# Optimization experiments

Measured on AMD Instinct MI355X. Metric: run time of the kernel, lower is better.

The kernel has to match this reference:

```python
import jax, jax.numpy as jnp
import numpy as np

N_NODES = 100000
N_EDGES = 1600000
IN_DIM = 128
HID = 64


def setup_inputs() -> dict:
    key = jax.random.key(0)
    ks = jax.random.split(key, 12)
    s = 1.0 / np.sqrt(IN_DIM)
    sh = 1.0 / np.sqrt(HID)
    return {
        "x": jax.random.normal(ks[0], (N_NODES, IN_DIM), jnp.float32),
        "edge_index": jax.random.randint(ks[1], (2, N_EDGES), 0, N_NODES, jnp.int64)
        if jax.config.jax_enable_x64 else jax.random.randint(ks[1], (2, N_EDGES), 0, N_NODES, jnp.int32),
        "edge_attr": jax.random.uniform(ks[2], (N_EDGES, 1), jnp.float32),
        "Wi": jax.random.normal(ks[3], (IN_DIM, HID), jnp.float32) * s,
        "bi": jnp.zeros((HID,), jnp.float32),
        "W1": jax.random.normal(ks[4], (HID, HID), jnp.float32) * sh,
        "b1": jnp.zeros((HID,), jnp.float32),
        "W2": jax.random.normal(ks[5], (HID, HID), jnp.float32) * sh,
        "b2": jnp.zeros((HID,), jnp.float32),
        "W3": jax.random.normal(ks[6], (HID, HID), jnp.float32) * sh,
        "b3": jnp.zeros((HID,), jnp.float32),
    }


def reference(x, edge_index, edge_attr, Wi, bi, W1, b1, W2, b2, W3, b3):
    src = edge_index[0]
    tgt = edge_index[1]
    w = edge_attr[:, 0:1]  # [E,1]
    h = jax.nn.relu(x @ Wi + bi)  # [N,H]
    states = [h]
    for W, b in ((W1, b1), (W2, b2), (W3, b3)):
        # per-edge weighted message, scatter-add into target nodes
        msgs = jax.ops.segment_sum(h[src] * w, tgt, num_segments=h.shape[0])
        h = jax.nn.relu((h + msgs) @ W + b)
        states.append(h)
    return jnp.stack(states)  # [4, N, H] (list of states in the original)
```

## Files before the change

### kernel.cpp

```cpp
#include <hip/hip_runtime.h>
#include <hip/hip_bf16.h>

#define N_NODES 100000
#define N_EDGES 1600000
#define IN_DIM  128
#define HID     64
#define CAP_N   64

#define PITCH_IN  152
#define PITCH_HID 88

typedef __attribute__((ext_vector_type(8))) short bf16x8;
typedef __attribute__((ext_vector_type(4))) float f32x4;

__device__ inline unsigned short f2bf(float f) {
    __hip_bfloat16 b = __float2bfloat16(f);
    return *reinterpret_cast<unsigned short*>(&b);
}

__global__ void wf_prep_kernel(const float* __restrict__ Wi,
                               const float* __restrict__ W1,
                               const float* __restrict__ W2,
                               const float* __restrict__ W3,
                               unsigned short* __restrict__ wf_in,
                               unsigned short* __restrict__ wf_hid,
                               int* __restrict__ cnt) {
    int t = blockIdx.x * 256 + threadIdx.x;
    if (t < N_NODES) cnt[t] = 0;
    if (t < 8192) {
        int j = t & 7, n16 = (t >> 3) & 15, quad = (t >> 7) & 3, nt = (t >> 9) & 3, kc = t >> 11;
        int k = kc * 32 + quad * 8 + j, n = nt * 16 + n16;
        wf_in[t] = f2bf(Wi[k * HID + n]);
    }
    if (t < 4096) {
        int j = t & 7, n16 = (t >> 3) & 15, quad = (t >> 7) & 3, nt = (t >> 9) & 3, kc = t >> 11;
        int k = kc * 32 + quad * 8 + j, n = nt * 16 + n16;
        wf_hid[t]        = f2bf(W1[k * HID + n]);
        wf_hid[4096 + t] = f2bf(W2[k * HID + n]);
        wf_hid[8192 + t] = f2bf(W3[k * HID + n]);
    }
}

__global__ __launch_bounds__(256) void scatter_direct_kernel(
        const int* __restrict__ src,
        const int* __restrict__ tgt,
        const float* __restrict__ ea,
        int* __restrict__ cnt,
        int2* __restrict__ binned) {
    int e = blockIdx.x * 256 + threadIdx.x;
    if (e < N_EDGES) {
        int t = tgt[e];
        int r = atomicAdd(&cnt[t], 1);
        if (r < CAP_N)
            binned[(size_t)t * CAP_N + r] = make_int2(src[e], __float_as_int(ea[e]));
    }
}

__global__ __launch_bounds__(256) void gemm_in_kernel(
        const float* __restrict__ x,
        const unsigned short* __restrict__ wf,
        const float* __restrict__ bi,
        float* __restrict__ h0,
        __hip_bfloat16* __restrict__ hbf) {
    __shared__ unsigned short sX[64 * PITCH_IN];
    const int tid  = threadIdx.x;
    const int row0 = blockIdx.x * 64;

    #pragma unroll
    for (int it = 0; it < 8; ++it) {
        int i  = tid + it * 256;
        int r  = i >> 5;
        int kq = i & 31;
        int rg = row0 + r;
        float4 v = (rg < N_NODES)
                 ? ((const float4*)x)[(size_t)rg * (IN_DIM / 4) + kq]
                 : make_float4(0.f, 0.f, 0.f, 0.f);
        ushort4 pk;
        pk.x = f2bf(v.x); pk.y = f2bf(v.y); pk.z = f2bf(v.z); pk.w = f2bf(v.w);
        *(ushort4*)(sX + r * PITCH_IN + kq * 4) = pk;
    }
    __syncthreads();

    const int lane = tid & 63;
    const int wid  = tid >> 6;
    const int l16  = lane & 15;
    const int q    = lane >> 4;

    f32x4 acc[4] = {{0,0,0,0},{0,0,0,0},{0,0,0,0},{0,0,0,0}};
    const bf16x8* wf8 = (const bf16x8*)wf;

    #pragma unroll
    for (int kc = 0; kc < 4; ++kc) {
        bf16x8 af = *(const bf16x8*)(sX + (wid * 16 + l16) * PITCH_IN + kc * 32 + q * 8);
        #pragma unroll
        for (int nt = 0; nt < 4; ++nt) {
            bf16x8 bfr = wf8[((kc * 4 + nt) * 4 + q) * 16 + l16];
            acc[nt] = __builtin_amdgcn_mfma_f32_16x16x32_bf16(af, bfr, acc[nt], 0, 0, 0);
        }
    }

    #pragma unroll
    for (int nt = 0; nt < 4; ++nt) {
        float bb = bi[nt * 16 + l16];
        #pragma unroll
        for (int reg = 0; reg < 4; ++reg) {
            int rg = row0 + wid * 16 + q * 4 + reg;
            if (rg < N_NODES) {
                float v = fmaxf(acc[nt][reg] + bb, 0.0f);
                h0 [(size_t)rg * HID + nt * 16 + l16] = v;
                hbf[(size_t)rg * HID + nt * 16 + l16] = __float2bfloat16(v);
            }
        }
    }
}

__global__ __launch_bounds__(256) void agg_gemm_kernel(
        const float* __restrict__ h,
        const __hip_bfloat16* __restrict__ hbf_in,
        const int* __restrict__ cnt,
        const int2* __restrict__ binned,
        const unsigned short* __restrict__ wf,
        const float* __restrict__ b,
        float* __restrict__ hnext,
        __hip_bfloat16* __restrict__ hbf_out,
        const int store_bf) {
    __shared__ unsigned short sXs[64 * PITCH_HID];
    const int tid  = threadIdx.x;
    const int row0 = blockIdx.x * 64;
    const int lane = tid & 63;
    const int wid  = tid >> 6;
    const int grp  = lane >> 4;
    const int sub  = lane & 15;

    const int node0 = row0 + wid * 16;

    int cv = 0;
    {
        int nl = node0 + (lane & 15);
        if (lane < 16 && nl < N_NODES) cv = min(cnt[nl], CAP_N);
    }

    int c0 = __shfl(cv, 0);
    int2 pl = binned[(size_t)min(node0, N_NODES - 1) * CAP_N + min(lane, max(c0 - 1, 0))];

    for (int t = 0; t < 16; ++t) {
        const int node = node0 + t;
        const int ccur = __shfl(cv, t);
        const int2 pl_cur = pl;
        if (t < 15) {
            int cn = __shfl(cv, t + 1);
            pl = binned[(size_t)min(node + 1, N_NODES - 1) * CAP_N
                        + min(lane, max(cn - 1, 0))];
        }
        if (node < N_NODES) {
            float ax = 0.f, ay = 0.f, az = 0.f, aw = 0.f;
            const int last = ccur - 1;
            for (int i = 0; i < ccur; i += 8) {
                int e0 = i + grp;
                int e1 = i + 4 + grp;
                bool l0 = (e0 <= last);
                bool l1 = (e1 <= last);
                int s0  = __shfl(pl_cur.x, l0 ? e0 : last);
                int w0i = __shfl(pl_cur.y, l0 ? e0 : last);
                int s1  = __shfl(pl_cur.x, l1 ? e1 : last);
                int w1i = __shfl(pl_cur.y, l1 ? e1 : last);
                uint2 g0 = *(const uint2*)(hbf_in + (size_t)s0 * HID + sub * 4);
                uint2 g1 = *(const uint2*)(hbf_in + (size_t)s1 * HID + sub * 4);
                float w0 = l0 ? __int_as_float(w0i) : 0.0f;
                float w1 = l1 ? __int_as_float(w1i) : 0.0f;
                ax += w0 * __uint_as_float(g0.x << 16);
                ay += w0 * __uint_as_float(g0.x & 0xFFFF0000u);
                az += w0 * __uint_as_float(g0.y << 16);
                aw += w0 * __uint_as_float(g0.y & 0xFFFF0000u);
                ax += w1 * __uint_as_float(g1.x << 16);
                ay += w1 * __uint_as_float(g1.x & 0xFFFF0000u);
                az += w1 * __uint_as_float(g1.y << 16);
                aw += w1 * __uint_as_float(g1.y & 0xFFFF0000u);
            }
            ax += __shfl_xor(ax, 16); ay += __shfl_xor(ay, 16);
            az += __shfl_xor(az, 16); aw += __shfl_xor(aw, 16);
            ax += __shfl_xor(ax, 32); ay += __shfl_xor(ay, 32);
            az += __shfl_xor(az, 32); aw += __shfl_xor(aw, 32);
            if (grp == 0) {
                const float4 hv = *(const float4*)(h + (size_t)node * HID + sub * 4);
                ushort4 pk;
                pk.x = f2bf(hv.x + ax); pk.y = f2bf(hv.y + ay);
                pk.z = f2bf(hv.z + az); pk.w = f2bf(hv.w + aw);
                *(ushort4*)(sXs + (wid * 16 + t) * PITCH_HID + sub * 4) = pk;
            }
        } else if (grp == 0) {
            ushort4 z; z.x = 0; z.y = 0; z.z = 0; z.w = 0;
            *(ushort4*)(sXs + (wid * 16 + t) * PITCH_HID + sub * 4) = z;
        }
    }
    __syncthreads();

    const int l16 = lane & 15;
    const int q   = lane >> 4;

    f32x4 acc[4] = {{0,0,0,0},{0,0,0,0},{0,0,0,0},{0,0,0,0}};
    const bf16x8* wf8 = (const bf16x8*)wf;

    #pragma unroll
    for (int kc = 0; kc < 2; ++kc) {
        bf16x8 af = *(const bf16x8*)(sXs + (wid * 16 + l16) * PITCH_HID + kc * 32 + q * 8);
        #pragma unroll
        for (int nt = 0; nt < 4; ++nt) {
            bf16x8 bfr = wf8[((kc * 4 + nt) * 4 + q) * 16 + l16];
            acc[nt] = __builtin_amdgcn_mfma_f32_16x16x32_bf16(af, bfr, acc[nt], 0, 0, 0);
        }
    }

    #pragma unroll
    for (int nt = 0; nt < 4; ++nt) {
        float bb = b[nt * 16 + l16];
        #pragma unroll
        for (int reg = 0; reg < 4; ++reg) {
            int rg = row0 + wid * 16 + q * 4 + reg;
            if (rg < N_NODES) {
                float v = fmaxf(acc[nt][reg] + bb, 0.0f);
                hnext[(size_t)rg * HID + nt * 16 + l16] = v;
                if (store_bf)
                    hbf_out[(size_t)rg * HID + nt * 16 + l16] = __float2bfloat16(v);
            }
        }
    }
}

extern "C" void kernel_launch(void* const* d_in, const int* in_sizes, int n_in,
                              void* d_out, int out_size, void* d_ws, size_t ws_size,
                              hipStream_t stream) {
    const float* x   = (const float*)d_in[0];
    const int*   ei  = (const int*)  d_in[1];
    const float* ea  = (const float*)d_in[2];
    const float* Wi  = (const float*)d_in[3];
    const float* bi  = (const float*)d_in[4];
    const float* W1  = (const float*)d_in[5];
    const float* b1  = (const float*)d_in[6];
    const float* W2  = (const float*)d_in[7];
    const float* b2  = (const float*)d_in[8];
    const float* W3  = (const float*)d_in[9];
    const float* b3  = (const float*)d_in[10];
    const float* bl[3] = { b1, b2, b3 };
    float* out = (float*)d_out;

    const int* src = ei;
    const int* tgt = ei + N_EDGES;

    int2* binned = (int2*)d_ws;
    int* cnt = (int*)(binned + (size_t)N_NODES * CAP_N);
    __hip_bfloat16* hbf0 = (__hip_bfloat16*)(cnt + N_NODES);
    __hip_bfloat16* hbf1 = hbf0 + (size_t)N_NODES * HID;
    unsigned short* wf_in  = (unsigned short*)(hbf1 + (size_t)N_NODES * HID);
    unsigned short* wf_hid = wf_in + 8192;

    const int prep_blocks = (N_NODES + 255) / 256;
    wf_prep_kernel<<<prep_blocks, 256, 0, stream>>>(Wi, W1, W2, W3,
                                                    wf_in, wf_hid, cnt);

    const int sc_blocks = (N_EDGES + 255) / 256;
    scatter_direct_kernel<<<sc_blocks, 256, 0, stream>>>(src, tgt, ea, cnt, binned);

    const int gemm_blocks = (N_NODES + 63) / 64;
    gemm_in_kernel<<<gemm_blocks, 256, 0, stream>>>(x, wf_in, bi, out, hbf0);

    __hip_bfloat16* hin  = hbf0;
    __hip_bfloat16* hout = hbf1;
    for (int l = 0; l < 3; ++l) {
        const float* hl = out + (size_t)l * N_NODES * HID;
        float* hn       = out + (size_t)(l + 1) * N_NODES * HID;
        agg_gemm_kernel<<<gemm_blocks, 256, 0, stream>>>(
            hl, hin, cnt, binned,
            wf_hid + (size_t)l * 4096, bl[l], hn, hout, (l < 2) ? 1 : 0);
        __hip_bfloat16* t = hin; hin = hout; hout = t;
    }
}
```

Measured before the change: 409.5 us.

## Fuse edge scatter with input GEMM and pad atomic counters

Merges the edge-binning scatter and the input projection GEMM into one launch. Even blocks bin 1024 edges each and odd blocks compute 64 rows of the GEMM, so the atomic-bound scatter can overlap with the bandwidth-bound GEMM. The per-node counters are spread to a 16-int stride so that atomics on neighbouring targets fall on separate cache lines. In exchange, the counter array grows, and the zeroing and later count reads become strided rather than contiguous.

```diff
diff --git a/kernel.cpp b/kernel.cpp
--- a/kernel.cpp
+++ b/kernel.cpp
@@ -6,6 +6,11 @@
 #define IN_DIM  128
 #define HID     64
 #define CAP_N   64
+#define CNT_STRIDE 16
+
+#define SC_EB   1024
+#define SC_BLOCKS ((N_EDGES + SC_EB - 1) / SC_EB)
+#define GEMM_BLOCKS ((N_NODES + 63) / 64)
 
 #define PITCH_IN  152
 #define PITCH_HID 88
@@ -26,7 +31,7 @@
                                unsigned short* __restrict__ wf_hid,
                                int* __restrict__ cnt) {
     int t = blockIdx.x * 256 + threadIdx.x;
-    if (t < N_NODES) cnt[t] = 0;
+    if (t < N_NODES) cnt[(size_t)t * CNT_STRIDE] = 0;
     if (t < 8192) {
         int j = t & 7, n16 = (t >> 3) & 15, quad = (t >> 7) & 3, nt = (t >> 9) & 3, kc = t >> 11;
         int k = kc * 32 + quad * 8 + j, n = nt * 16 + n16;
@@ -41,30 +46,38 @@
     }
 }
 
-__global__ __launch_bounds__(256) void scatter_direct_kernel(
+__global__ __launch_bounds__(256) void fused_scatter_gemm_kernel(
         const int* __restrict__ src,
         const int* __restrict__ tgt,
         const float* __restrict__ ea,
         int* __restrict__ cnt,
-        int2* __restrict__ binned) {
-    int e = blockIdx.x * 256 + threadIdx.x;
-    if (e < N_EDGES) {
-        int t = tgt[e];
-        int r = atomicAdd(&cnt[t], 1);
-        if (r < CAP_N)
-            binned[(size_t)t * CAP_N + r] = make_int2(src[e], __float_as_int(ea[e]));
-    }
-}
-
-__global__ __launch_bounds__(256) void gemm_in_kernel(
+        int2* __restrict__ binned,
         const float* __restrict__ x,
         const unsigned short* __restrict__ wf,
         const float* __restrict__ bi,
         float* __restrict__ h0,
         __hip_bfloat16* __restrict__ hbf) {
     __shared__ unsigned short sX[64 * PITCH_IN];
-    const int tid  = threadIdx.x;
-    const int row0 = blockIdx.x * 64;
+    const int tid = threadIdx.x;
+
+    if ((blockIdx.x & 1) == 0) {
+        const int s  = blockIdx.x >> 1;
+        const int e0 = s * SC_EB;
+        #pragma unroll
+        for (int k = 0; k < SC_EB / 256; ++k) {
+            int e = e0 + tid + k * 256;
+            if (e < N_EDGES) {
+                int t = tgt[e];
+                int r = atomicAdd(&cnt[(size_t)t * CNT_STRIDE], 1);
+                if (r < CAP_N)
+                    binned[(size_t)t * CAP_N + r] =
+                        make_int2(src[e], __float_as_int(ea[e]));
+            }
+        }
+        return;
+    }
+
+    const int row0 = (blockIdx.x >> 1) * 64;
 
     #pragma unroll
     for (int it = 0; it < 8; ++it) {
@@ -137,7 +150,8 @@
     int cv = 0;
     {
         int nl = node0 + (lane & 15);
-        if (lane < 16 && nl < N_NODES) cv = min(cnt[nl], CAP_N);
+        if (lane < 16 && nl < N_NODES)
+            cv = min(cnt[(size_t)nl * CNT_STRIDE], CAP_N);
     }
 
     int c0 = __shfl(cv, 0);
@@ -249,7 +263,7 @@
 
     int2* binned = (int2*)d_ws;
     int* cnt = (int*)(binned + (size_t)N_NODES * CAP_N);
-    __hip_bfloat16* hbf0 = (__hip_bfloat16*)(cnt + N_NODES);
+    __hip_bfloat16* hbf0 = (__hip_bfloat16*)(cnt + (size_t)N_NODES * CNT_STRIDE);
     __hip_bfloat16* hbf1 = hbf0 + (size_t)N_NODES * HID;
     unsigned short* wf_in  = (unsigned short*)(hbf1 + (size_t)N_NODES * HID);
     unsigned short* wf_hid = wf_in + 8192;
@@ -258,18 +272,15 @@
     wf_prep_kernel<<<prep_blocks, 256, 0, stream>>>(Wi, W1, W2, W3,
                                                     wf_in, wf_hid, cnt);
 
-    const int sc_blocks = (N_EDGES + 255) / 256;
-    scatter_direct_kernel<<<sc_blocks, 256, 0, stream>>>(src, tgt, ea, cnt, binned);
-
-    const int gemm_blocks = (N_NODES + 63) / 64;
-    gemm_in_kernel<<<gemm_blocks, 256, 0, stream>>>(x, wf_in, bi, out, hbf0);
+    fused_scatter_gemm_kernel<<<SC_BLOCKS + GEMM_BLOCKS, 256, 0, stream>>>(
+        src, tgt, ea, cnt, binned, x, wf_in, bi, out, hbf0);
 
     __hip_bfloat16* hin  = hbf0;
     __hip_bfloat16* hout = hbf1;
     for (int l = 0; l < 3; ++l) {
         const float* hl = out + (size_t)l * N_NODES * HID;
         float* hn       = out + (size_t)(l + 1) * N_NODES * HID;
-        agg_gemm_kernel<<<gemm_blocks, 256, 0, stream>>>(
+        agg_gemm_kernel<<<GEMM_BLOCKS, 256, 0, stream>>>(
             hl, hin, cnt, binned,
             wf_hid + (size_t)l * 4096, bl[l], hn, hout, (l < 2) ? 1 : 0);
         __hip_bfloat16* t = hin; hin = hout; hout = t;
```

Measured after the change: 397.7 us. 2.9% less time.
